# Kernel tuning notes

Hardware: AMD Instinct MI355X
Metric: run time of the kernel (lower is better)

## Reference

```python
import jax, jax.numpy as jnp
import numpy as np

B = 4096  # number of rows (batch of 1-D sequences)
N = 4096  # transform length


def setup_inputs() -> dict:
    key = jax.random.key(0)
    x = jax.random.normal(key, (B, N), dtype=jnp.float32)
    # get_expk(N): expk[k] = (cos(pi*k/(2N)), -sin(pi*k/(2N)))
    t = jnp.arange(N, dtype=jnp.float32) * (np.pi / (2.0 * N))
    expk = jnp.stack([jnp.cos(t), -jnp.sin(t)], axis=-1)  # [N, 2]
    return {"x": x, "expk": expk}


def reference(x, expk):
    # IDCT (DCT-III), 2N-point FFT formulation:
    #   y_k = x_0 + 2 * sum_{n=1}^{N-1} x_n cos(pi*n*(2k+1)/(2N))
    #       = Re{ sum_n w_n x_n exp(j*pi*n/(2N)) * exp(j*2*pi*n*k/(2N)) },  w_0=1, w_n=2
    # i.e. the first N outputs of a 2N-point inverse DFT of the zero-padded,
    # twiddle-premultiplied sequence.
    n = x.shape[-1]
    # expk stores (cos(theta), -sin(theta)) => exp(+j*theta) = expk0 - j*expk1
    coef = (expk[..., 0] - 1j * expk[..., 1]).astype(jnp.complex64)  # [N]
    w = jnp.concatenate([jnp.ones((1,), x.dtype), jnp.full((n - 1,), 2.0, x.dtype)])
    a = (x * w).astype(jnp.complex64) * coef                      # [B, N]
    A = jnp.concatenate([a, jnp.zeros_like(a)], axis=-1)          # [B, 2N] zero-pad
    y = jnp.real(jnp.fft.ifft(A, axis=-1))[..., :n] * (2.0 * n)   # undo 1/(2N) of ifft
    return y.astype(x.dtype)
```

## Files before the change

### kernel.cpp

```cpp
#include <hip/hip_runtime.h>


#define NFFT 4096
#define NT   256
#define PADIDX(i) ((i) + ((i) >> 4))
#define PADN  (NFFT + (NFFT >> 4))

__device__ __forceinline__ void cmul(float ar, float ai, float br, float bi,
                                     float& orr, float& oii) {
    orr = ar * br - ai * bi;
    oii = ar * bi + ai * br;
}

__device__ __forceinline__ void dft16(float vr[16], float vi[16]) {
    constexpr float WR[4][4] = {
        {1.f, 1.f, 1.f, 1.f},
        {1.f,  0.92387953251128674f,  0.70710678118654752f,  0.38268343236508977f},
        {1.f,  0.70710678118654752f,  0.f,                  -0.70710678118654752f},
        {1.f,  0.38268343236508977f, -0.70710678118654752f, -0.92387953251128674f}};
    constexpr float WI[4][4] = {
        {0.f, 0.f, 0.f, 0.f},
        {0.f,  0.38268343236508977f,  0.70710678118654752f,  0.92387953251128674f},
        {0.f,  0.70710678118654752f,  1.f,                   0.70710678118654752f},
        {0.f,  0.92387953251128674f,  0.70710678118654752f, -0.38268343236508977f}};
    float ur[16], ui[16];
#pragma unroll
    for (int p = 0; p < 4; ++p) {
        float apcr = vr[p] + vr[p + 8],      apci = vi[p] + vi[p + 8];
        float amcr = vr[p] - vr[p + 8],      amci = vi[p] - vi[p + 8];
        float bpdr = vr[p + 4] + vr[p + 12], bpdi = vi[p + 4] + vi[p + 12];
        float bmdr = vr[p + 4] - vr[p + 12], bmdi = vi[p + 4] - vi[p + 12];
        float y0r = apcr + bpdr, y0i = apci + bpdi;
        float y1r = amcr - bmdi, y1i = amci + bmdr;
        float y2r = apcr - bpdr, y2i = apci - bpdi;
        float y3r = amcr + bmdi, y3i = amci - bmdr;
        ur[4 * p + 0] = y0r;  ui[4 * p + 0] = y0i;
        cmul(y1r, y1i, WR[p][1], WI[p][1], ur[4 * p + 1], ui[4 * p + 1]);
        cmul(y2r, y2i, WR[p][2], WI[p][2], ur[4 * p + 2], ui[4 * p + 2]);
        cmul(y3r, y3i, WR[p][3], WI[p][3], ur[4 * p + 3], ui[4 * p + 3]);
    }
#pragma unroll
    for (int q = 0; q < 4; ++q) {
        float apcr = ur[q] + ur[q + 8],      apci = ui[q] + ui[q + 8];
        float amcr = ur[q] - ur[q + 8],      amci = ui[q] - ui[q + 8];
        float bpdr = ur[q + 4] + ur[q + 12], bpdi = ui[q + 4] + ui[q + 12];
        float bmdr = ur[q + 4] - ur[q + 12], bmdi = ui[q + 4] - ui[q + 12];
        vr[q]      = apcr + bpdr;  vi[q]      = apci + bpdi;
        vr[q + 4]  = amcr - bmdi;  vi[q + 4]  = amci + bmdr;
        vr[q + 8]  = apcr - bpdr;  vi[q + 8]  = apci - bpdi;
        vr[q + 12] = amcr + bmdi;  vi[q + 12] = amci - bmdr;
    }
}

__device__ __forceinline__ void twiddle_apply(float vr[16], float vi[16],
                                              float w1r, float w1i) {
    float cr = w1r, ci = w1i;
#pragma unroll
    for (int r = 1; r < 16; ++r) {
        float tr, ti;
        cmul(vr[r], vi[r], cr, ci, tr, ti);
        vr[r] = tr; vi[r] = ti;
        if (r < 15) {
            float nr, ni;
            cmul(cr, ci, w1r, w1i, nr, ni);
            cr = nr; ci = ni;
        }
    }
}

extern "C" __global__ void __launch_bounds__(NT, 3)
idct_fft_kernel(const float* __restrict__ x, const float* __restrict__ expk,
                float* __restrict__ out)
{
    __shared__ float Sr[PADN], Si[PADN];
    __shared__ float Twr[NFFT / 4], Twi[NFFT / 4];

    const int tid = threadIdx.x;
    const long row = blockIdx.x;
    const float* __restrict__ xrow = x + row * (long)NFFT;
    const float2* __restrict__ e2 = (const float2*)expk;

#pragma unroll
    for (int j = 0; j < 4; ++j) {
        int r = tid + NT * j;
        float2 e = e2[4 * r];
        Twr[r] = e.x;
        Twi[r] = -e.y;
    }

    float vr[16], vi[16];
#pragma unroll
    for (int j = 0; j < 16; ++j) {
        int n = tid + NT * j;
        float xv = xrow[n];
        float2 e = e2[n];
        float w = (n == 0) ? 1.0f : 2.0f;
        vr[j] = w * xv * e.x;
        vi[j] = -(w * xv * e.y);
    }
    __syncthreads();
    dft16(vr, vi);
    twiddle_apply(vr, vi, Twr[tid], Twi[tid]);
#pragma unroll
    for (int r = 0; r < 16; ++r) {
        int a = PADIDX(16 * tid + r);
        Sr[a] = vr[r]; Si[a] = vi[r];
    }
    __syncthreads();

#pragma unroll
    for (int j = 0; j < 16; ++j) {
        int a = PADIDX(tid + NT * j);
        vr[j] = Sr[a]; vi[j] = Si[a];
    }
    __syncthreads();
    dft16(vr, vi);
    {
        int e = tid & ~15;
        twiddle_apply(vr, vi, Twr[e], Twi[e]);
    }
    {
        int ba = (tid & 15) + 16 * (tid & ~15);
#pragma unroll
        for (int r = 0; r < 16; ++r) {
            int a = PADIDX(ba + 16 * r);
            Sr[a] = vr[r]; Si[a] = vi[r];
        }
    }
    __syncthreads();

#pragma unroll
    for (int j = 0; j < 16; ++j) {
        int a = PADIDX(tid + NT * j);
        vr[j] = Sr[a]; vi[j] = Si[a];
    }
    __syncthreads();
    dft16(vr, vi);
#pragma unroll
    for (int r = 0; r < 16; ++r) {
        Sr[PADIDX(tid + NT * r)] = vr[r];
    }
    __syncthreads();

    float2* __restrict__ y2 = (float2*)(out + row * (long)NFFT);
#pragma unroll
    for (int t = 0; t < 8; ++t) {
        int m = tid + NT * t;
        float a = Sr[PADIDX(m)];
        float b = Sr[PADIDX(NFFT - 1 - m)];
        y2[m] = make_float2(a, b);
    }
}

extern "C" void kernel_launch(void* const* d_in, const int* in_sizes, int n_in,
                              void* d_out, int out_size, void* d_ws, size_t ws_size,
                              hipStream_t stream) {
    const float* x    = (const float*)d_in[0];
    const float* expk = (const float*)d_in[1];
    float* out        = (float*)d_out;
    const int nrows   = in_sizes[0] / NFFT;
    hipLaunchKernelGGL(idct_fft_kernel, dim3(nrows), dim3(NT), 0, stream,
                       x, expk, out);
}
```

Before: 126.3 us.

## Use swizzled interleaved complex LDS layout, drop twiddle table, raise occupancy

Replaces the padded split real/imag shared arrays with one interleaved float2 array addressed through an XOR swizzle. The first-stage write becomes 16-byte vector stores. The shared twiddle table is removed and twiddles are read straight from expk in global memory, which also drops one barrier. Shared memory per block falls from about 42 KB to 32 KB, and launch bounds rise from 3 to 5 blocks per CU to increase occupancy. The risks are register spills under the tighter launch bound, possible bank conflicts in the swizzle pattern, and extra global loads for the twiddles.

```diff
diff --git a/kernel.cpp b/kernel.cpp
--- a/kernel.cpp
+++ b/kernel.cpp
@@ -3,8 +3,7 @@
 
 #define NFFT 4096
 #define NT   256
-#define PADIDX(i) ((i) + ((i) >> 4))
-#define PADN  (NFFT + (NFFT >> 4))
+#define SWZ(p) ((p) ^ (((p) >> 3) & 0xE))
 
 __device__ __forceinline__ void cmul(float ar, float ai, float br, float bi,
                                      float& orr, float& oii) {
@@ -68,25 +67,17 @@
     }
 }
 
-extern "C" __global__ void __launch_bounds__(NT, 3)
+extern "C" __global__ void __launch_bounds__(NT, 5)
 idct_fft_kernel(const float* __restrict__ x, const float* __restrict__ expk,
                 float* __restrict__ out)
 {
-    __shared__ float Sr[PADN], Si[PADN];
-    __shared__ float Twr[NFFT / 4], Twi[NFFT / 4];
+    __shared__ __align__(16) float2 S[NFFT];
+    float* __restrict__ Sf = (float*)S;
 
     const int tid = threadIdx.x;
     const long row = blockIdx.x;
     const float* __restrict__ xrow = x + row * (long)NFFT;
     const float2* __restrict__ e2 = (const float2*)expk;
-
-#pragma unroll
-    for (int j = 0; j < 4; ++j) {
-        int r = tid + NT * j;
-        float2 e = e2[4 * r];
-        Twr[r] = e.x;
-        Twi[r] = -e.y;
-    }
 
     float vr[16], vi[16];
 #pragma unroll
@@ -98,47 +89,49 @@
         vr[j] = w * xv * e.x;
         vi[j] = -(w * xv * e.y);
     }
-    __syncthreads();
     dft16(vr, vi);
-    twiddle_apply(vr, vi, Twr[tid], Twi[tid]);
+    {
+        float2 we = e2[4 * tid];
+        twiddle_apply(vr, vi, we.x, -we.y);
+    }
 #pragma unroll
-    for (int r = 0; r < 16; ++r) {
-        int a = PADIDX(16 * tid + r);
-        Sr[a] = vr[r]; Si[a] = vi[r];
+    for (int rp = 0; rp < 8; ++rp) {
+        int p = 16 * tid + 2 * rp;
+        float4 st = make_float4(vr[2 * rp], vi[2 * rp], vr[2 * rp + 1], vi[2 * rp + 1]);
+        *(float4*)&S[SWZ(p)] = st;
     }
     __syncthreads();
 
 #pragma unroll
     for (int j = 0; j < 16; ++j) {
-        int a = PADIDX(tid + NT * j);
-        vr[j] = Sr[a]; vi[j] = Si[a];
+        float2 c = S[SWZ(tid + NT * j)];
+        vr[j] = c.x; vi[j] = c.y;
     }
     __syncthreads();
     dft16(vr, vi);
     {
-        int e = tid & ~15;
-        twiddle_apply(vr, vi, Twr[e], Twi[e]);
+        float2 we = e2[64 * (tid >> 4)];
+        twiddle_apply(vr, vi, we.x, -we.y);
     }
     {
-        int ba = (tid & 15) + 16 * (tid & ~15);
+        int ba = (tid & 15) + ((tid >> 4) << 8);
 #pragma unroll
         for (int r = 0; r < 16; ++r) {
-            int a = PADIDX(ba + 16 * r);
-            Sr[a] = vr[r]; Si[a] = vi[r];
+            S[SWZ(ba + 16 * r)] = make_float2(vr[r], vi[r]);
         }
     }
     __syncthreads();
 
 #pragma unroll
     for (int j = 0; j < 16; ++j) {
-        int a = PADIDX(tid + NT * j);
-        vr[j] = Sr[a]; vi[j] = Si[a];
+        float2 c = S[SWZ(tid + NT * j)];
+        vr[j] = c.x; vi[j] = c.y;
     }
     __syncthreads();
     dft16(vr, vi);
 #pragma unroll
     for (int r = 0; r < 16; ++r) {
-        Sr[PADIDX(tid + NT * r)] = vr[r];
+        Sf[tid + NT * r] = vr[r];
     }
     __syncthreads();
 
@@ -146,8 +139,8 @@
 #pragma unroll
     for (int t = 0; t < 8; ++t) {
         int m = tid + NT * t;
-        float a = Sr[PADIDX(m)];
-        float b = Sr[PADIDX(NFFT - 1 - m)];
+        float a = Sf[m];
+        float b = Sf[NFFT - 1 - m];
         y2[m] = make_float2(a, b);
     }
 }
```

Result: slower. 144.4 us (+14.3%).
